# Kernel tuning notes

Measured on AMD Instinct MI355X. Metric: run time of the kernel, lower is better.

## Reference

```python
import jax, jax.numpy as jnp
import numpy as np

B, T, E = 4, 2048, 1024
H, D = 16, 64

def setup_inputs() -> dict:
    key = jax.random.key(0)
    k0, k1, k2, k3 = jax.random.split(key, 4)
    x = jax.random.normal(k0, (B, T, E), dtype=jnp.float32)
    Wq = jax.random.normal(k1, (H, E, D), dtype=jnp.float32) * (E ** -0.5)
    Wk = jax.random.normal(k2, (H, E, D), dtype=jnp.float32) * (E ** -0.5)
    Wv = jax.random.normal(k3, (H, E, D), dtype=jnp.float32) * (E ** -0.5)
    return {"x": x, "Wq": Wq, "Wk": Wk, "Wv": Wv}

def reference(x, Wq, Wk, Wv):
    # per-head projections: [B,T,E] x [H,E,D] -> [B,H,T,D]
    q = jnp.einsum('bte,hed->bhtd', x, Wq)
    k = jnp.einsum('bte,hed->bhtd', x, Wk)
    v = jnp.einsum('bte,hed->bhtd', x, Wv)
    d = q.shape[-1]
    scores = jnp.einsum('bhtd,bhsd->bhts', q, k) / jnp.sqrt(jnp.asarray(d, q.dtype))
    Tlen = x.shape[1]
    causal = jnp.tril(jnp.ones((Tlen, Tlen), dtype=bool))
    scores = jnp.where(causal, scores, -jnp.inf)
    weights = jax.nn.softmax(scores, axis=-1)
    out = jnp.einsum('bhts,bhsd->bhtd', weights, v)  # [B,H,T,D]
    # concat heads along last dim (head order preserved like torch.cat)
    Bb, Hh, Tt, Dd = out.shape
    return out.transpose(0, 2, 1, 3).reshape(Bb, Tt, Hh * Dd)
```

## Files before the change

kernel.cpp:

```cpp
#include <hip/hip_runtime.h>
#include <hip/hip_bf16.h>

#define BATCH 4
#define SEQ   2048
#define EMB   1024
#define NH    16
#define HD    64

#define Q_OFF  ((size_t)0)
#define K_OFF  ((size_t)8388608)
#define V_OFF  ((size_t)16777216)
#define WT_OFF ((size_t)25165824)

typedef __attribute__((ext_vector_type(8))) short short8;
typedef __attribute__((ext_vector_type(4))) short short4v;
typedef __attribute__((ext_vector_type(4))) float f32x4;

__device__ __forceinline__ short8 pack8s(float4 a, float4 b, float s) {
    alignas(16) __hip_bfloat16 t[8] = {
        __float2bfloat16(a.x * s), __float2bfloat16(a.y * s),
        __float2bfloat16(a.z * s), __float2bfloat16(a.w * s),
        __float2bfloat16(b.x * s), __float2bfloat16(b.y * s),
        __float2bfloat16(b.z * s), __float2bfloat16(b.w * s)};
    return *reinterpret_cast<const short8*>(t);
}

__device__ __forceinline__ void async16(void* lds, const void* g) {
    __builtin_amdgcn_global_load_lds(
        (const __attribute__((address_space(1))) unsigned int*)g,
        (__attribute__((address_space(3))) unsigned int*)lds, 16, 0, 0);
}

__global__ __launch_bounds__(256)
void xcast_kernel(const float* __restrict__ x, __hip_bfloat16* __restrict__ xb)
{
    const size_t i = ((size_t)blockIdx.x * 256 + threadIdx.x) * 8;
    float4 f0 = ((const float4*)(x + i))[0];
    float4 f1 = ((const float4*)(x + i))[1];
    *(short8*)(xb + i) = pack8s(f0, f1, 1.0f);
}

__global__ __launch_bounds__(256)
void wt_kernel(const float* __restrict__ Wq, const float* __restrict__ Wk,
               const float* __restrict__ Wv, __hip_bfloat16* __restrict__ Wt)
{
    const int et = blockIdx.x;
    const int mh = blockIdx.y;
    const int m = mh >> 4, h = mh & 15;
    const float* W = ((m == 0) ? Wq : (m == 1) ? Wk : Wv) + (size_t)h * (EMB * HD);
    const float scale = (m == 0) ? 0.18033688011112042f : 1.0f;

    __shared__ __hip_bfloat16 T[64][72];
    const int tid = threadIdx.x;
    const int r   = tid >> 2;
    const int seg = (tid & 3) * 16;

    {
        const float* src = W + (size_t)(et * 64 + r) * HD + seg;
        float4 f0 = ((const float4*)src)[0];
        float4 f1 = ((const float4*)src)[1];
        float4 f2 = ((const float4*)src)[2];
        float4 f3 = ((const float4*)src)[3];
        const float v[16] = {f0.x,f0.y,f0.z,f0.w, f1.x,f1.y,f1.z,f1.w,
                             f2.x,f2.y,f2.z,f2.w, f3.x,f3.y,f3.z,f3.w};
        #pragma unroll
        for (int j = 0; j < 16; ++j) T[seg + j][r] = __float2bfloat16(v[j] * scale);
    }
    __syncthreads();
    __hip_bfloat16* dst = Wt + ((size_t)mh * HD + r) * EMB + et * 64 + seg;
    *(short8*)dst       = *(const short8*)&T[r][seg];
    *(short8*)(dst + 8) = *(const short8*)&T[r][seg + 8];
}

__global__ __launch_bounds__(256)
void qkv_proj_kernel(const __hip_bfloat16* __restrict__ xb,
                     const __hip_bfloat16* __restrict__ Wt,
                     __hip_bfloat16* __restrict__ qkv)
{
    const int nt = blockIdx.x;
    const int rt = blockIdx.y;
    const int row0 = rt * 128;
    const int n0   = nt * 128;

    __shared__ __hip_bfloat16 lds[17408];
    __hip_bfloat16* As = lds;
    __hip_bfloat16* Bs = lds + 8192;

    const int tid  = threadIdx.x;
    const int wave = tid >> 6;
    const int lane = tid & 63;
    const int lr   = lane & 15;
    const int lg   = lane >> 4;

    const int srow  = lane >> 3;
    const int sslot = (lane & 7) ^ srow;
    const char* aSrc = (const char*)xb + (size_t)(row0 + wave * 32 + srow) * 2048 + sslot * 16;
    const char* bSrc = (const char*)Wt + (size_t)(n0   + wave * 32 + srow) * 2048 + sslot * 16;
    char* aDst = (char*)As + (size_t)(wave * 32) * 128;
    char* bDst = (char*)Bs + (size_t)(wave * 32) * 128;

    f32x4 acc[2][8] = {};

    for (int k0 = 0; k0 < EMB; k0 += 64) {
        __syncthreads();
        #pragma unroll
        for (int i = 0; i < 4; ++i) {
            async16(aDst + i * 1024, aSrc + (size_t)i * 16384 + k0 * 2);
            async16(bDst + i * 1024, bSrc + (size_t)i * 16384 + k0 * 2);
        }
        __syncthreads();

        #pragma unroll
        for (int half = 0; half < 2; ++half) {
            const int cg = half * 4 + lg;
            const int r0a = wave * 32 + lr;
            const int r1a = wave * 32 + 16 + lr;
            short8 a0 = *(const short8*)((char*)As + r0a * 128 + ((cg ^ (r0a & 7)) * 16));
            short8 a1 = *(const short8*)((char*)As + r1a * 128 + ((cg ^ (r1a & 7)) * 16));
            #pragma unroll
            for (int ct = 0; ct < 8; ++ct) {
                const int rb = ct * 16 + lr;
                short8 bf = *(const short8*)((char*)Bs + rb * 128 + ((cg ^ (rb & 7)) * 16));
                acc[0][ct] = __builtin_amdgcn_mfma_f32_16x16x32_bf16(a0, bf, acc[0][ct], 0, 0, 0);
                acc[1][ct] = __builtin_amdgcn_mfma_f32_16x16x32_bf16(a1, bf, acc[1][ct], 0, 0, 0);
            }
        }
    }

    const int m   = n0 >> 10;
    const int b   = row0 >> 11;
    const int tl0 = (row0 & (SEQ - 1)) + wave * 32;
    if (m < 2) {
        __hip_bfloat16* outp = qkv + ((m == 0) ? Q_OFF : K_OFF)
                             + (size_t)b * NH * SEQ * HD;
        #pragma unroll
        for (int rsub = 0; rsub < 2; ++rsub)
            #pragma unroll
            for (int ct = 0; ct < 8; ++ct) {
                const int h = (2 * nt + (ct >> 2)) & 15;
                const int d = (ct & 3) * 16 + lr;
                #pragma unroll
                for (int i = 0; i < 4; ++i) {
                    const int trow = tl0 + rsub * 16 + lg * 4 + i;
                    outp[((size_t)h * SEQ + trow) * HD + d] = __float2bfloat16(acc[rsub][ct][i]);
                }
            }
    } else {
        __hip_bfloat16 (*Ts)[136] = (__hip_bfloat16(*)[136])lds;
        __syncthreads();
        #pragma unroll
        for (int rsub = 0; rsub < 2; ++rsub)
            #pragma unroll
            for (int ct = 0; ct < 8; ++ct)
                #pragma unroll
                for (int i = 0; i < 4; ++i)
                    Ts[ct * 16 + lr][wave * 32 + rsub * 16 + lg * 4 + i] =
                        __float2bfloat16(acc[rsub][ct][i]);
        __syncthreads();
        const int c    = tid >> 1;
        const int tseg = (tid & 1) * 64;
        const int hv   = (2 * nt + (c >> 6)) & 15;
        const int dv   = c & 63;
        __hip_bfloat16* dst = qkv + V_OFF + ((size_t)b * NH + hv) * (HD * SEQ)
                            + (size_t)dv * SEQ + (row0 & (SEQ - 1)) + tseg;
        #pragma unroll
        for (int q = 0; q < 8; ++q)
            *(short8*)(dst + q * 8) = *(const short8*)&Ts[c][tseg + q * 8];
    }
}

__global__ __launch_bounds__(256)
void attn_kernel(const __hip_bfloat16* __restrict__ ws, float* __restrict__ out)
{
    const int bid     = blockIdx.x;
    const int logical = (bid & 7) * 64 + (bid >> 3);
    const int p  = logical & 7;
    const int h  = (logical >> 3) & 15;
    const int b  = logical >> 7;

    const __hip_bfloat16* qp = ws + Q_OFF + ((size_t)b * NH + h) * (SEQ * HD);
    const __hip_bfloat16* kp = ws + K_OFF + ((size_t)b * NH + h) * (SEQ * HD);
    const __hip_bfloat16* vt = ws + V_OFF + ((size_t)b * NH + h) * (HD * SEQ);

    __shared__ __align__(16) __hip_bfloat16 Ksb[2][4096];
    __shared__ __align__(16) __hip_bfloat16 Vsb[2][4096];
    __shared__ __align__(16) __hip_bfloat16 Psb[4][1024];

    const int tid  = threadIdx.x;
    const int wave = tid >> 6;
    const int lane = tid & 63;
    const int lr   = lane & 15;
    const int lg   = lane >> 4;
    const int l7   = lr & 7;

    const int srow8 = lane >> 3;
    const int sslot = (lane & 7) ^ srow8;

    float* op = out + (size_t)b * SEQ * (NH * HD) + (size_t)h * HD;

    for (int seg = 0; seg < 2; ++seg) {
        const int qt    = seg ? (15 - p) : p;
        const int qbase = qt * 128;
        const int ktmax = 2 * qt + 1;

        short8 qf[2][2];
        #pragma unroll
        for (int rsub = 0; rsub < 2; ++rsub) {
            const __hip_bfloat16* src =
                qp + (size_t)(qbase + wave * 32 + rsub * 16 + lr) * HD + lg * 8;
            qf[rsub][0] = *(const short8*)src;
            qf[rsub][1] = *(const short8*)(src + 32);
        }

        float m_run[2] = {-1e30f, -1e30f};
        float l_run[2] = {0.f, 0.f};
        f32x4 o_acc[2][4] = {};

        auto stage = [&](int buf, int kbase) {
            #pragma unroll
            for (int j = 0; j < 2; ++j) {
                const int r0 = wave * 16 + j * 8;
                async16((char*)Ksb[buf] + r0 * 128,
                        (const char*)(kp + (size_t)(kbase + r0 + srow8) * HD) + sslot * 16);
                async16((char*)Vsb[buf] + r0 * 128,
                        (const char*)(vt + (size_t)(r0 + srow8) * SEQ + kbase) + sslot * 16);
            }
        };

        stage(0, 0);
        __syncthreads();

        for (int kt = 0; kt <= ktmax; ++kt) {
            const int cur = kt & 1;
            if (kt < ktmax) stage(cur ^ 1, (kt + 1) * 64);

            f32x4 s[2][4];
            __builtin_amdgcn_s_setprio(1);
            #pragma unroll
            for (int ct = 0; ct < 4; ++ct) {
                const char* kb = (const char*)Ksb[cur] + (ct * 16 + lr) * 128;
                short8 kf0 = *(const short8*)(kb + ((lg      ^ l7) << 4));
                short8 kf1 = *(const short8*)(kb + (((lg + 4) ^ l7) << 4));
                #pragma unroll
                for (int rsub = 0; rsub < 2; ++rsub) {
                    f32x4 z = {};
                    z           = __builtin_amdgcn_mfma_f32_16x16x32_bf16(kf0, qf[rsub][0], z, 0, 0, 0);
                    s[rsub][ct] = __builtin_amdgcn_mfma_f32_16x16x32_bf16(kf1, qf[rsub][1], z, 0, 0, 0);
                }
            }
            __builtin_amdgcn_s_setprio(0);

            const int kbase = kt * 64;
            if (kt >= 2 * qt) {
                #pragma unroll
                for (int rsub = 0; rsub < 2; ++rsub) {
                    const int qrow = qbase + wave * 32 + rsub * 16 + lr;
                    #pragma unroll
                    for (int ct = 0; ct < 4; ++ct)
                        #pragma unroll
                        for (int i = 0; i < 4; ++i) {
                            const int key = kbase + ct * 16 + lg * 4 + i;
                            s[rsub][ct][i] = (key > qrow) ? -1e30f : s[rsub][ct][i];
                        }
                }
            }

            #pragma unroll
            for (int rsub = 0; rsub < 2; ++rsub) {
                float pmax = fmaxf(
                    fmaxf(fmaxf(fmaxf(s[rsub][0][0], s[rsub][0][1]), fmaxf(s[rsub][0][2], s[rsub][0][3])),
                          fmaxf(fmaxf(s[rsub][1][0], s[rsub][1][1]), fmaxf(s[rsub][1][2], s[rsub][1][3]))),
                    fmaxf(fmaxf(fmaxf(s[rsub][2][0], s[rsub][2][1]), fmaxf(s[rsub][2][2], s[rsub][2][3])),
                          fmaxf(fmaxf(s[rsub][3][0], s[rsub][3][1]), fmaxf(s[rsub][3][2], s[rsub][3][3]))));
                pmax = fmaxf(pmax, __shfl_xor(pmax, 16, 64));
                pmax = fmaxf(pmax, __shfl_xor(pmax, 32, 64));

                if (__any(pmax > m_run[rsub] + 8.0f)) {
                    const float mnew = fmaxf(m_run[rsub], pmax);
                    const float corr = __builtin_amdgcn_exp2f(m_run[rsub] - mnew);
                    l_run[rsub] *= corr;
                    #pragma unroll
                    for (int ct = 0; ct < 4; ++ct)
                        #pragma unroll
                        for (int i = 0; i < 4; ++i)
                            o_acc[rsub][ct][i] *= corr;
                    m_run[rsub] = mnew;
                }

                const float mcur = m_run[rsub];
                float rs0 = 0.f, rs1 = 0.f;
                #pragma unroll
                for (int ct = 0; ct < 4; ++ct) {
                    const float p0 = __builtin_amdgcn_exp2f(s[rsub][ct][0] - mcur);
                    const float p1 = __builtin_amdgcn_exp2f(s[rsub][ct][1] - mcur);
                    const float p2 = __builtin_amdgcn_exp2f(s[rsub][ct][2] - mcur);
                    const float p3 = __builtin_amdgcn_exp2f(s[rsub][ct][3] - mcur);
                    rs0 += p0 + p1;
                    rs1 += p2 + p3;
                    alignas(8) __hip_bfloat16 t[4] = {
                        __float2bfloat16(p0), __float2bfloat16(p1),
                        __float2bfloat16(p2), __float2bfloat16(p3)};
                    *(short4v*)((char*)Psb[wave] + lr * 128
                        + (((2 * ct + (lg >> 1)) ^ l7) << 4) + 8 * (lg & 1)) = *(const short4v*)t;
                }
                float rs = rs0 + rs1;
                rs += __shfl_xor(rs, 16, 64);
                rs += __shfl_xor(rs, 32, 64);
                l_run[rsub] += rs;

                const char* pb = (const char*)Psb[wave] + lr * 128;
                short8 pf0 = *(const short8*)(pb + ((lg      ^ l7) << 4));
                short8 pf1 = *(const short8*)(pb + (((lg + 4) ^ l7) << 4));
                __builtin_amdgcn_s_setprio(1);
                #pragma unroll
                for (int ct = 0; ct < 4; ++ct) {
                    const char* vb = (const char*)Vsb[cur] + (ct * 16 + lr) * 128;
                    short8 vf0 = *(const short8*)(vb + ((lg      ^ l7) << 4));
                    short8 vf1 = *(const short8*)(vb + (((lg + 4) ^ l7) << 4));
                    o_acc[rsub][ct] = __builtin_amdgcn_mfma_f32_16x16x32_bf16(vf0, pf0, o_acc[rsub][ct], 0, 0, 0);
                    o_acc[rsub][ct] = __builtin_amdgcn_mfma_f32_16x16x32_bf16(vf1, pf1, o_acc[rsub][ct], 0, 0, 0);
                }
                __builtin_amdgcn_s_setprio(0);
            }

            __syncthreads();
        }

        #pragma unroll
        for (int rsub = 0; rsub < 2; ++rsub) {
            const float inv  = 1.0f / l_run[rsub];
            const int   trow = qbase + wave * 32 + rsub * 16 + lr;
            #pragma unroll
            for (int ct = 0; ct < 4; ++ct) {
                float4 o;
                o.x = o_acc[rsub][ct][0] * inv;
                o.y = o_acc[rsub][ct][1] * inv;
                o.z = o_acc[rsub][ct][2] * inv;
                o.w = o_acc[rsub][ct][3] * inv;
                *(float4*)&op[(size_t)trow * (NH * HD) + ct * 16 + lg * 4] = o;
            }
        }
    }
}

extern "C" void kernel_launch(void* const* d_in, const int* in_sizes, int n_in,
                              void* d_out, int out_size, void* d_ws, size_t ws_size,
                              hipStream_t stream) {
    const float* x  = (const float*)d_in[0];
    const float* Wq = (const float*)d_in[1];
    const float* Wk = (const float*)d_in[2];
    const float* Wv = (const float*)d_in[3];
    float* out = (float*)d_out;
    __hip_bfloat16* ws = (__hip_bfloat16*)d_ws;

    __hip_bfloat16* xb = (__hip_bfloat16*)d_out;

    hipLaunchKernelGGL(xcast_kernel, dim3((BATCH * SEQ * EMB) / (256 * 8)), dim3(256),
                       0, stream, x, xb);
    hipLaunchKernelGGL(wt_kernel, dim3(16, 48), dim3(256), 0, stream,
                       Wq, Wk, Wv, ws + WT_OFF);
    hipLaunchKernelGGL(qkv_proj_kernel, dim3(24, 64), dim3(256), 0, stream,
                       xb, ws + WT_OFF, ws);
    hipLaunchKernelGGL(attn_kernel, dim3(512), dim3(256), 0, stream, ws, out);
}
```

Baseline: 157.3 us.

## Load K/V fragments directly from global memory and give each block one query tile

The attention kernel drops the double-buffered LDS staging of K and V tiles and the per-tile __syncthreads. Each wave now loads its MFMA fragments straight from global memory into registers. The grid doubles to 1024 blocks, each handling a single 128-row query tile with the longest tiles scheduled first, replacing the paired short/long segment scheme. This removes block-wide barriers and LDS traffic, but each wave now issues redundant global/L2 loads of the same K/V data, latency is no longer hidden by async prefetch, and register pressure rises.

Measured after the change: 261.6 us. 1.66x slower.

```diff
diff --git a/kernel.cpp b/kernel.cpp
--- a/kernel.cpp
+++ b/kernel.cpp
@@ -173,18 +173,19 @@
 void attn_kernel(const __hip_bfloat16* __restrict__ ws, float* __restrict__ out)
 {
     const int bid     = blockIdx.x;
-    const int logical = (bid & 7) * 64 + (bid >> 3);
-    const int p  = logical & 7;
-    const int h  = (logical >> 3) & 15;
-    const int b  = logical >> 7;
-
-    const __hip_bfloat16* qp = ws + Q_OFF + ((size_t)b * NH + h) * (SEQ * HD);
-    const __hip_bfloat16* kp = ws + K_OFF + ((size_t)b * NH + h) * (SEQ * HD);
-    const __hip_bfloat16* vt = ws + V_OFF + ((size_t)b * NH + h) * (HD * SEQ);
-
-    __shared__ __align__(16) __hip_bfloat16 Ksb[2][4096];
-    __shared__ __align__(16) __hip_bfloat16 Vsb[2][4096];
-    __shared__ __align__(16) __hip_bfloat16 Psb[4][1024];
+    const int logical = (bid & 7) * 128 + (bid >> 3);
+    const int qt = 15 - (logical & 15);
+    const int bh = logical >> 4;
+    const int h  = bh & 15;
+    const int b  = bh >> 4;
+    const int qbase = qt * 128;
+    const int ktmax = 2 * qt + 1;
+
+    const __hip_bfloat16* qp = ws + Q_OFF + (size_t)bh * (SEQ * HD);
+    const __hip_bfloat16* kp = ws + K_OFF + (size_t)bh * (SEQ * HD);
+    const __hip_bfloat16* vt = ws + V_OFF + (size_t)bh * (HD * SEQ);
+
+    __shared__ __align__(16) __hip_bfloat16 Psb[4][2][1024];
 
     const int tid  = threadIdx.x;
     const int wave = tid >> 6;
@@ -193,152 +194,142 @@
     const int lg   = lane >> 4;
     const int l7   = lr & 7;
 
-    const int srow8 = lane >> 3;
-    const int sslot = (lane & 7) ^ srow8;
+    short8 qf[2][2];
+    #pragma unroll
+    for (int rsub = 0; rsub < 2; ++rsub) {
+        const __hip_bfloat16* src =
+            qp + (size_t)(qbase + wave * 32 + rsub * 16 + lr) * HD + lg * 8;
+        qf[rsub][0] = *(const short8*)src;
+        qf[rsub][1] = *(const short8*)(src + 32);
+    }
+
+    float m_run[2] = {-1e30f, -1e30f};
+    float l_run[2] = {0.f, 0.f};
+    f32x4 o_acc[2][4] = {};
+
+    const __hip_bfloat16* kfp = kp + (size_t)(lr) * HD + lg * 8;
+    const __hip_bfloat16* vfp = vt + (size_t)(lr) * SEQ + lg * 8;
+
+    for (int kt = 0; kt <= ktmax; ++kt) {
+        const int kbase = kt * 64;
+
+        short8 kf[4][2];
+        #pragma unroll
+        for (int ct = 0; ct < 4; ++ct) {
+            const __hip_bfloat16* kb = kfp + (size_t)(kbase + ct * 16) * HD;
+            kf[ct][0] = *(const short8*)kb;
+            kf[ct][1] = *(const short8*)(kb + 32);
+        }
+
+        f32x4 s[2][4];
+        __builtin_amdgcn_s_setprio(1);
+        #pragma unroll
+        for (int ct = 0; ct < 4; ++ct)
+            #pragma unroll
+            for (int rsub = 0; rsub < 2; ++rsub) {
+                f32x4 z = {};
+                z           = __builtin_amdgcn_mfma_f32_16x16x32_bf16(kf[ct][0], qf[rsub][0], z, 0, 0, 0);
+                s[rsub][ct] = __builtin_amdgcn_mfma_f32_16x16x32_bf16(kf[ct][1], qf[rsub][1], z, 0, 0, 0);
+            }
+        __builtin_amdgcn_s_setprio(0);
+
+        short8 vf[4][2];
+        #pragma unroll
+        for (int ct = 0; ct < 4; ++ct) {
+            const __hip_bfloat16* vb = vfp + (size_t)(ct * 16) * SEQ + kbase;
+            vf[ct][0] = *(const short8*)vb;
+            vf[ct][1] = *(const short8*)(vb + 32);
+        }
+
+        if (kt >= 2 * qt) {
+            #pragma unroll
+            for (int rsub = 0; rsub < 2; ++rsub) {
+                const int qrow = qbase + wave * 32 + rsub * 16 + lr;
+                #pragma unroll
+                for (int ct = 0; ct < 4; ++ct)
+                    #pragma unroll
+                    for (int i = 0; i < 4; ++i) {
+                        const int key = kbase + ct * 16 + lg * 4 + i;
+                        s[rsub][ct][i] = (key > qrow) ? -1e30f : s[rsub][ct][i];
+                    }
+            }
+        }
+
+        #pragma unroll
+        for (int rsub = 0; rsub < 2; ++rsub) {
+            float pmax = fmaxf(
+                fmaxf(fmaxf(fmaxf(s[rsub][0][0], s[rsub][0][1]), fmaxf(s[rsub][0][2], s[rsub][0][3])),
+                      fmaxf(fmaxf(s[rsub][1][0], s[rsub][1][1]), fmaxf(s[rsub][1][2], s[rsub][1][3]))),
+                fmaxf(fmaxf(fmaxf(s[rsub][2][0], s[rsub][2][1]), fmaxf(s[rsub][2][2], s[rsub][2][3])),
+                      fmaxf(fmaxf(s[rsub][3][0], s[rsub][3][1]), fmaxf(s[rsub][3][2], s[rsub][3][3]))));
+            pmax = fmaxf(pmax, __shfl_xor(pmax, 16, 64));
+            pmax = fmaxf(pmax, __shfl_xor(pmax, 32, 64));
+
+            if (__any(pmax > m_run[rsub] + 8.0f)) {
+                const float mnew = fmaxf(m_run[rsub], pmax);
+                const float corr = __builtin_amdgcn_exp2f(m_run[rsub] - mnew);
+                l_run[rsub] *= corr;
+                #pragma unroll
+                for (int ct = 0; ct < 4; ++ct)
+                    #pragma unroll
+                    for (int i = 0; i < 4; ++i)
+                        o_acc[rsub][ct][i] *= corr;
+                m_run[rsub] = mnew;
+            }
+
+            const float mcur = m_run[rsub];
+            float rs0 = 0.f, rs1 = 0.f;
+            #pragma unroll
+            for (int ct = 0; ct < 4; ++ct) {
+                const float p0 = __builtin_amdgcn_exp2f(s[rsub][ct][0] - mcur);
+                const float p1 = __builtin_amdgcn_exp2f(s[rsub][ct][1] - mcur);
+                const float p2 = __builtin_amdgcn_exp2f(s[rsub][ct][2] - mcur);
+                const float p3 = __builtin_amdgcn_exp2f(s[rsub][ct][3] - mcur);
+                rs0 += p0 + p1;
+                rs1 += p2 + p3;
+                alignas(8) __hip_bfloat16 t[4] = {
+                    __float2bfloat16(p0), __float2bfloat16(p1),
+                    __float2bfloat16(p2), __float2bfloat16(p3)};
+                *(short4v*)((char*)Psb[wave][rsub] + lr * 128
+                    + (((2 * ct + (lg >> 1)) ^ l7) << 4) + 8 * (lg & 1)) = *(const short4v*)t;
+            }
+            float rs = rs0 + rs1;
+            rs += __shfl_xor(rs, 16, 64);
+            rs += __shfl_xor(rs, 32, 64);
+            l_run[rsub] += rs;
+        }
+
+        short8 pf[2][2];
+        #pragma unroll
+        for (int rsub = 0; rsub < 2; ++rsub) {
+            const char* pb = (const char*)Psb[wave][rsub] + lr * 128;
+            pf[rsub][0] = *(const short8*)(pb + ((lg      ^ l7) << 4));
+            pf[rsub][1] = *(const short8*)(pb + (((lg + 4) ^ l7) << 4));
+        }
+        __builtin_amdgcn_s_setprio(1);
+        #pragma unroll
+        for (int ct = 0; ct < 4; ++ct)
+            #pragma unroll
+            for (int rsub = 0; rsub < 2; ++rsub) {
+                o_acc[rsub][ct] = __builtin_amdgcn_mfma_f32_16x16x32_bf16(vf[ct][0], pf[rsub][0], o_acc[rsub][ct], 0, 0, 0);
+                o_acc[rsub][ct] = __builtin_amdgcn_mfma_f32_16x16x32_bf16(vf[ct][1], pf[rsub][1], o_acc[rsub][ct], 0, 0, 0);
+            }
+        __builtin_amdgcn_s_setprio(0);
+    }
 
     float* op = out + (size_t)b * SEQ * (NH * HD) + (size_t)h * HD;
-
-    for (int seg = 0; seg < 2; ++seg) {
-        const int qt    = seg ? (15 - p) : p;
-        const int qbase = qt * 128;
-        const int ktmax = 2 * qt + 1;
-
-        short8 qf[2][2];
-        #pragma unroll
-        for (int rsub = 0; rsub < 2; ++rsub) {
-            const __hip_bfloat16* src =
-                qp + (size_t)(qbase + wave * 32 + rsub * 16 + lr) * HD + lg * 8;
-            qf[rsub][0] = *(const short8*)src;
-            qf[rsub][1] = *(const short8*)(src + 32);
-        }
-
-        float m_run[2] = {-1e30f, -1e30f};
-        float l_run[2] = {0.f, 0.f};
-        f32x4 o_acc[2][4] = {};
-
-        auto stage = [&](int buf, int kbase) {
-            #pragma unroll
-            for (int j = 0; j < 2; ++j) {
-                const int r0 = wave * 16 + j * 8;
-                async16((char*)Ksb[buf] + r0 * 128,
-                        (const char*)(kp + (size_t)(kbase + r0 + srow8) * HD) + sslot * 16);
-                async16((char*)Vsb[buf] + r0 * 128,
-                        (const char*)(vt + (size_t)(r0 + srow8) * SEQ + kbase) + sslot * 16);
-            }
-        };
-
-        stage(0, 0);
-        __syncthreads();
-
-        for (int kt = 0; kt <= ktmax; ++kt) {
-            const int cur = kt & 1;
-            if (kt < ktmax) stage(cur ^ 1, (kt + 1) * 64);
-
-            f32x4 s[2][4];
-            __builtin_amdgcn_s_setprio(1);
-            #pragma unroll
-            for (int ct = 0; ct < 4; ++ct) {
-                const char* kb = (const char*)Ksb[cur] + (ct * 16 + lr) * 128;
-                short8 kf0 = *(const short8*)(kb + ((lg      ^ l7) << 4));
-                short8 kf1 = *(const short8*)(kb + (((lg + 4) ^ l7) << 4));
-                #pragma unroll
-                for (int rsub = 0; rsub < 2; ++rsub) {
-                    f32x4 z = {};
-                    z           = __builtin_amdgcn_mfma_f32_16x16x32_bf16(kf0, qf[rsub][0], z, 0, 0, 0);
-                    s[rsub][ct] = __builtin_amdgcn_mfma_f32_16x16x32_bf16(kf1, qf[rsub][1], z, 0, 0, 0);
-                }
-            }
-            __builtin_amdgcn_s_setprio(0);
-
-            const int kbase = kt * 64;
-            if (kt >= 2 * qt) {
-                #pragma unroll
-                for (int rsub = 0; rsub < 2; ++rsub) {
-                    const int qrow = qbase + wave * 32 + rsub * 16 + lr;
-                    #pragma unroll
-                    for (int ct = 0; ct < 4; ++ct)
-                        #pragma unroll
-                        for (int i = 0; i < 4; ++i) {
-                            const int key = kbase + ct * 16 + lg * 4 + i;
-                            s[rsub][ct][i] = (key > qrow) ? -1e30f : s[rsub][ct][i];
-                        }
-                }
-            }
-
-            #pragma unroll
-            for (int rsub = 0; rsub < 2; ++rsub) {
-                float pmax = fmaxf(
-                    fmaxf(fmaxf(fmaxf(s[rsub][0][0], s[rsub][0][1]), fmaxf(s[rsub][0][2], s[rsub][0][3])),
-                          fmaxf(fmaxf(s[rsub][1][0], s[rsub][1][1]), fmaxf(s[rsub][1][2], s[rsub][1][3]))),
-                    fmaxf(fmaxf(fmaxf(s[rsub][2][0], s[rsub][2][1]), fmaxf(s[rsub][2][2], s[rsub][2][3])),
-                          fmaxf(fmaxf(s[rsub][3][0], s[rsub][3][1]), fmaxf(s[rsub][3][2], s[rsub][3][3]))));
-                pmax = fmaxf(pmax, __shfl_xor(pmax, 16, 64));
-                pmax = fmaxf(pmax, __shfl_xor(pmax, 32, 64));
-
-                if (__any(pmax > m_run[rsub] + 8.0f)) {
-                    const float mnew = fmaxf(m_run[rsub], pmax);
-                    const float corr = __builtin_amdgcn_exp2f(m_run[rsub] - mnew);
-                    l_run[rsub] *= corr;
-                    #pragma unroll
-                    for (int ct = 0; ct < 4; ++ct)
-                        #pragma unroll
-                        for (int i = 0; i < 4; ++i)
-                            o_acc[rsub][ct][i] *= corr;
-                    m_run[rsub] = mnew;
-                }
-
-                const float mcur = m_run[rsub];
-                float rs0 = 0.f, rs1 = 0.f;
-                #pragma unroll
-                for (int ct = 0; ct < 4; ++ct) {
-                    const float p0 = __builtin_amdgcn_exp2f(s[rsub][ct][0] - mcur);
-                    const float p1 = __builtin_amdgcn_exp2f(s[rsub][ct][1] - mcur);
-                    const float p2 = __builtin_amdgcn_exp2f(s[rsub][ct][2] - mcur);
-                    const float p3 = __builtin_amdgcn_exp2f(s[rsub][ct][3] - mcur);
-                    rs0 += p0 + p1;
-                    rs1 += p2 + p3;
-                    alignas(8) __hip_bfloat16 t[4] = {
-                        __float2bfloat16(p0), __float2bfloat16(p1),
-                        __float2bfloat16(p2), __float2bfloat16(p3)};
-                    *(short4v*)((char*)Psb[wave] + lr * 128
-                        + (((2 * ct + (lg >> 1)) ^ l7) << 4) + 8 * (lg & 1)) = *(const short4v*)t;
-                }
-                float rs = rs0 + rs1;
-                rs += __shfl_xor(rs, 16, 64);
-                rs += __shfl_xor(rs, 32, 64);
-                l_run[rsub] += rs;
-
-                const char* pb = (const char*)Psb[wave] + lr * 128;
-                short8 pf0 = *(const short8*)(pb + ((lg      ^ l7) << 4));
-                short8 pf1 = *(const short8*)(pb + (((lg + 4) ^ l7) << 4));
-                __builtin_amdgcn_s_setprio(1);
-                #pragma unroll
-                for (int ct = 0; ct < 4; ++ct) {
-                    const char* vb = (const char*)Vsb[cur] + (ct * 16 + lr) * 128;
-                    short8 vf0 = *(const short8*)(vb + ((lg      ^ l7) << 4));
-                    short8 vf1 = *(const short8*)(vb + (((lg + 4) ^ l7) << 4));
-                    o_acc[rsub][ct] = __builtin_amdgcn_mfma_f32_16x16x32_bf16(vf0, pf0, o_acc[rsub][ct], 0, 0, 0);
-                    o_acc[rsub][ct] = __builtin_amdgcn_mfma_f32_16x16x32_bf16(vf1, pf1, o_acc[rsub][ct], 0, 0, 0);
-                }
-                __builtin_amdgcn_s_setprio(0);
-            }
-
-            __syncthreads();
-        }
-
-        #pragma unroll
-        for (int rsub = 0; rsub < 2; ++rsub) {
-            const float inv  = 1.0f / l_run[rsub];
-            const int   trow = qbase + wave * 32 + rsub * 16 + lr;
-            #pragma unroll
-            for (int ct = 0; ct < 4; ++ct) {
-                float4 o;
-                o.x = o_acc[rsub][ct][0] * inv;
-                o.y = o_acc[rsub][ct][1] * inv;
-                o.z = o_acc[rsub][ct][2] * inv;
-                o.w = o_acc[rsub][ct][3] * inv;
-                *(float4*)&op[(size_t)trow * (NH * HD) + ct * 16 + lg * 4] = o;
-            }
+    #pragma unroll
+    for (int rsub = 0; rsub < 2; ++rsub) {
+        const float inv  = 1.0f / l_run[rsub];
+        const int   trow = qbase + wave * 32 + rsub * 16 + lr;
+        #pragma unroll
+        for (int ct = 0; ct < 4; ++ct) {
+            float4 o;
+            o.x = o_acc[rsub][ct][0] * inv;
+            o.y = o_acc[rsub][ct][1] * inv;
+            o.z = o_acc[rsub][ct][2] * inv;
+            o.w = o_acc[rsub][ct][3] * inv;
+            *(float4*)&op[(size_t)trow * (NH * HD) + ct * 16 + lg * 4] = o;
         }
     }
 }
@@ -361,5 +352,5 @@
                        Wq, Wk, Wv, ws + WT_OFF);
     hipLaunchKernelGGL(qkv_proj_kernel, dim3(24, 64), dim3(256), 0, stream,
                        xb, ws + WT_OFF, ws);
-    hipLaunchKernelGGL(attn_kernel, dim3(512), dim3(256), 0, stream, ws, out);
-}
+    hipLaunchKernelGGL(attn_kernel, dim3(1024), dim3(256), 0, stream, ws, out);
+}
```

## Launch one attention block per query tile, heaviest first, and batch PV MFMAs

Applied to the files above, without the earlier changes.

Replaces the paired-segment scheme (each of 512 blocks processing two complementary query tiles) with 1024 blocks, each handling one 128-row query tile. Tiles are ordered longest-first so the hardware scheduler can balance the causal workload dynamically. The P tile is now staged per rsub, so both rows' PV MFMAs run together and each V fragment loaded from LDS is reused twice. This adds more block launches and doubles the per-wave P buffer in LDS, which may reduce occupancy.

After: 182.8 us. 16.2% more time.

```diff
diff --git a/kernel.cpp b/kernel.cpp
--- a/kernel.cpp
+++ b/kernel.cpp
@@ -173,18 +173,21 @@
 void attn_kernel(const __hip_bfloat16* __restrict__ ws, float* __restrict__ out)
 {
     const int bid     = blockIdx.x;
-    const int logical = (bid & 7) * 64 + (bid >> 3);
-    const int p  = logical & 7;
-    const int h  = (logical >> 3) & 15;
-    const int b  = logical >> 7;
-
-    const __hip_bfloat16* qp = ws + Q_OFF + ((size_t)b * NH + h) * (SEQ * HD);
-    const __hip_bfloat16* kp = ws + K_OFF + ((size_t)b * NH + h) * (SEQ * HD);
-    const __hip_bfloat16* vt = ws + V_OFF + ((size_t)b * NH + h) * (HD * SEQ);
+    const int logical = (bid & 7) * 128 + (bid >> 3);
+    const int qt = 15 - (logical & 15);
+    const int bh = logical >> 4;
+    const int h  = bh & 15;
+    const int b  = bh >> 4;
+    const int qbase = qt * 128;
+    const int ktmax = 2 * qt + 1;
+
+    const __hip_bfloat16* qp = ws + Q_OFF + (size_t)bh * (SEQ * HD);
+    const __hip_bfloat16* kp = ws + K_OFF + (size_t)bh * (SEQ * HD);
+    const __hip_bfloat16* vt = ws + V_OFF + (size_t)bh * (HD * SEQ);
 
     __shared__ __align__(16) __hip_bfloat16 Ksb[2][4096];
     __shared__ __align__(16) __hip_bfloat16 Vsb[2][4096];
-    __shared__ __align__(16) __hip_bfloat16 Psb[4][1024];
+    __shared__ __align__(16) __hip_bfloat16 Psb[4][2][1024];
 
     const int tid  = threadIdx.x;
     const int wave = tid >> 6;
@@ -196,149 +199,149 @@
     const int srow8 = lane >> 3;
     const int sslot = (lane & 7) ^ srow8;
 
+    short8 qf[2][2];
+    #pragma unroll
+    for (int rsub = 0; rsub < 2; ++rsub) {
+        const __hip_bfloat16* src =
+            qp + (size_t)(qbase + wave * 32 + rsub * 16 + lr) * HD + lg * 8;
+        qf[rsub][0] = *(const short8*)src;
+        qf[rsub][1] = *(const short8*)(src + 32);
+    }
+
+    float m_run[2] = {-1e30f, -1e30f};
+    float l_run[2] = {0.f, 0.f};
+    f32x4 o_acc[2][4] = {};
+
+    auto stage = [&](int buf, int kbase) {
+        #pragma unroll
+        for (int j = 0; j < 2; ++j) {
+            const int r0 = wave * 16 + j * 8;
+            async16((char*)Ksb[buf] + r0 * 128,
+                    (const char*)(kp + (size_t)(kbase + r0 + srow8) * HD) + sslot * 16);
+            async16((char*)Vsb[buf] + r0 * 128,
+                    (const char*)(vt + (size_t)(r0 + srow8) * SEQ + kbase) + sslot * 16);
+        }
+    };
+
+    stage(0, 0);
+    __syncthreads();
+
+    for (int kt = 0; kt <= ktmax; ++kt) {
+        const int cur = kt & 1;
+        if (kt < ktmax) stage(cur ^ 1, (kt + 1) * 64);
+
+        f32x4 s[2][4];
+        __builtin_amdgcn_s_setprio(1);
+        #pragma unroll
+        for (int ct = 0; ct < 4; ++ct) {
+            const char* kb = (const char*)Ksb[cur] + (ct * 16 + lr) * 128;
+            short8 kf0 = *(const short8*)(kb + ((lg      ^ l7) << 4));
+            short8 kf1 = *(const short8*)(kb + (((lg + 4) ^ l7) << 4));
+            #pragma unroll
+            for (int rsub = 0; rsub < 2; ++rsub) {
+                f32x4 z = {};
+                z           = __builtin_amdgcn_mfma_f32_16x16x32_bf16(kf0, qf[rsub][0], z, 0, 0, 0);
+                s[rsub][ct] = __builtin_amdgcn_mfma_f32_16x16x32_bf16(kf1, qf[rsub][1], z, 0, 0, 0);
+            }
+        }
+        __builtin_amdgcn_s_setprio(0);
+
+        const int kbase = kt * 64;
+        if (kt >= 2 * qt) {
+            #pragma unroll
+            for (int rsub = 0; rsub < 2; ++rsub) {
+                const int qrow = qbase + wave * 32 + rsub * 16 + lr;
+                #pragma unroll
+                for (int ct = 0; ct < 4; ++ct)
+                    #pragma unroll
+                    for (int i = 0; i < 4; ++i) {
+                        const int key = kbase + ct * 16 + lg * 4 + i;
+                        s[rsub][ct][i] = (key > qrow) ? -1e30f : s[rsub][ct][i];
+                    }
+            }
+        }
+
+        #pragma unroll
+        for (int rsub = 0; rsub < 2; ++rsub) {
+            float pmax = fmaxf(
+                fmaxf(fmaxf(fmaxf(s[rsub][0][0], s[rsub][0][1]), fmaxf(s[rsub][0][2], s[rsub][0][3])),
+                      fmaxf(fmaxf(s[rsub][1][0], s[rsub][1][1]), fmaxf(s[rsub][1][2], s[rsub][1][3]))),
+                fmaxf(fmaxf(fmaxf(s[rsub][2][0], s[rsub][2][1]), fmaxf(s[rsub][2][2], s[rsub][2][3])),
+                      fmaxf(fmaxf(s[rsub][3][0], s[rsub][3][1]), fmaxf(s[rsub][3][2], s[rsub][3][3]))));
+            pmax = fmaxf(pmax, __shfl_xor(pmax, 16, 64));
+            pmax = fmaxf(pmax, __shfl_xor(pmax, 32, 64));
+
+            if (__any(pmax > m_run[rsub] + 8.0f)) {
+                const float mnew = fmaxf(m_run[rsub], pmax);
+                const float corr = __builtin_amdgcn_exp2f(m_run[rsub] - mnew);
+                l_run[rsub] *= corr;
+                #pragma unroll
+                for (int ct = 0; ct < 4; ++ct)
+                    #pragma unroll
+                    for (int i = 0; i < 4; ++i)
+                        o_acc[rsub][ct][i] *= corr;
+                m_run[rsub] = mnew;
+            }
+
+            const float mcur = m_run[rsub];
+            float rs0 = 0.f, rs1 = 0.f;
+            #pragma unroll
+            for (int ct = 0; ct < 4; ++ct) {
+                const float p0 = __builtin_amdgcn_exp2f(s[rsub][ct][0] - mcur);
+                const float p1 = __builtin_amdgcn_exp2f(s[rsub][ct][1] - mcur);
+                const float p2 = __builtin_amdgcn_exp2f(s[rsub][ct][2] - mcur);
+                const float p3 = __builtin_amdgcn_exp2f(s[rsub][ct][3] - mcur);
+                rs0 += p0 + p1;
+                rs1 += p2 + p3;
+                alignas(8) __hip_bfloat16 t[4] = {
+                    __float2bfloat16(p0), __float2bfloat16(p1),
+                    __float2bfloat16(p2), __float2bfloat16(p3)};
+                *(short4v*)((char*)Psb[wave][rsub] + lr * 128
+                    + (((2 * ct + (lg >> 1)) ^ l7) << 4) + 8 * (lg & 1)) = *(const short4v*)t;
+            }
+            float rs = rs0 + rs1;
+            rs += __shfl_xor(rs, 16, 64);
+            rs += __shfl_xor(rs, 32, 64);
+            l_run[rsub] += rs;
+        }
+
+        short8 pf[2][2];
+        #pragma unroll
+        for (int rsub = 0; rsub < 2; ++rsub) {
+            const char* pb = (const char*)Psb[wave][rsub] + lr * 128;
+            pf[rsub][0] = *(const short8*)(pb + ((lg      ^ l7) << 4));
+            pf[rsub][1] = *(const short8*)(pb + (((lg + 4) ^ l7) << 4));
+        }
+        __builtin_amdgcn_s_setprio(1);
+        #pragma unroll
+        for (int ct = 0; ct < 4; ++ct) {
+            const char* vb = (const char*)Vsb[cur] + (ct * 16 + lr) * 128;
+            short8 vf0 = *(const short8*)(vb + ((lg      ^ l7) << 4));
+            short8 vf1 = *(const short8*)(vb + (((lg + 4) ^ l7) << 4));
+            #pragma unroll
+            for (int rsub = 0; rsub < 2; ++rsub) {
+                o_acc[rsub][ct] = __builtin_amdgcn_mfma_f32_16x16x32_bf16(vf0, pf[rsub][0], o_acc[rsub][ct], 0, 0, 0);
+                o_acc[rsub][ct] = __builtin_amdgcn_mfma_f32_16x16x32_bf16(vf1, pf[rsub][1], o_acc[rsub][ct], 0, 0, 0);
+            }
+        }
+        __builtin_amdgcn_s_setprio(0);
+
+        __syncthreads();
+    }
+
     float* op = out + (size_t)b * SEQ * (NH * HD) + (size_t)h * HD;
-
-    for (int seg = 0; seg < 2; ++seg) {
-        const int qt    = seg ? (15 - p) : p;
-        const int qbase = qt * 128;
-        const int ktmax = 2 * qt + 1;
-
-        short8 qf[2][2];
-        #pragma unroll
-        for (int rsub = 0; rsub < 2; ++rsub) {
-            const __hip_bfloat16* src =
-                qp + (size_t)(qbase + wave * 32 + rsub * 16 + lr) * HD + lg * 8;
-            qf[rsub][0] = *(const short8*)src;
-            qf[rsub][1] = *(const short8*)(src + 32);
-        }
-
-        float m_run[2] = {-1e30f, -1e30f};
-        float l_run[2] = {0.f, 0.f};
-        f32x4 o_acc[2][4] = {};
-
-        auto stage = [&](int buf, int kbase) {
-            #pragma unroll
-            for (int j = 0; j < 2; ++j) {
-                const int r0 = wave * 16 + j * 8;
-                async16((char*)Ksb[buf] + r0 * 128,
-                        (const char*)(kp + (size_t)(kbase + r0 + srow8) * HD) + sslot * 16);
-                async16((char*)Vsb[buf] + r0 * 128,
-                        (const char*)(vt + (size_t)(r0 + srow8) * SEQ + kbase) + sslot * 16);
-            }
-        };
-
-        stage(0, 0);
-        __syncthreads();
-
-        for (int kt = 0; kt <= ktmax; ++kt) {
-            const int cur = kt & 1;
-            if (kt < ktmax) stage(cur ^ 1, (kt + 1) * 64);
-
-            f32x4 s[2][4];
-            __builtin_amdgcn_s_setprio(1);
-            #pragma unroll
-            for (int ct = 0; ct < 4; ++ct) {
-                const char* kb = (const char*)Ksb[cur] + (ct * 16 + lr) * 128;
-                short8 kf0 = *(const short8*)(kb + ((lg      ^ l7) << 4));
-                short8 kf1 = *(const short8*)(kb + (((lg + 4) ^ l7) << 4));
-                #pragma unroll
-                for (int rsub = 0; rsub < 2; ++rsub) {
-                    f32x4 z = {};
-                    z           = __builtin_amdgcn_mfma_f32_16x16x32_bf16(kf0, qf[rsub][0], z, 0, 0, 0);
-                    s[rsub][ct] = __builtin_amdgcn_mfma_f32_16x16x32_bf16(kf1, qf[rsub][1], z, 0, 0, 0);
-                }
-            }
-            __builtin_amdgcn_s_setprio(0);
-
-            const int kbase = kt * 64;
-            if (kt >= 2 * qt) {
-                #pragma unroll
-                for (int rsub = 0; rsub < 2; ++rsub) {
-                    const int qrow = qbase + wave * 32 + rsub * 16 + lr;
-                    #pragma unroll
-                    for (int ct = 0; ct < 4; ++ct)
-                        #pragma unroll
-                        for (int i = 0; i < 4; ++i) {
-                            const int key = kbase + ct * 16 + lg * 4 + i;
-                            s[rsub][ct][i] = (key > qrow) ? -1e30f : s[rsub][ct][i];
-                        }
-                }
-            }
-
-            #pragma unroll
-            for (int rsub = 0; rsub < 2; ++rsub) {
-                float pmax = fmaxf(
-                    fmaxf(fmaxf(fmaxf(s[rsub][0][0], s[rsub][0][1]), fmaxf(s[rsub][0][2], s[rsub][0][3])),
-                          fmaxf(fmaxf(s[rsub][1][0], s[rsub][1][1]), fmaxf(s[rsub][1][2], s[rsub][1][3]))),
-                    fmaxf(fmaxf(fmaxf(s[rsub][2][0], s[rsub][2][1]), fmaxf(s[rsub][2][2], s[rsub][2][3])),
-                          fmaxf(fmaxf(s[rsub][3][0], s[rsub][3][1]), fmaxf(s[rsub][3][2], s[rsub][3][3]))));
-                pmax = fmaxf(pmax, __shfl_xor(pmax, 16, 64));
-                pmax = fmaxf(pmax, __shfl_xor(pmax, 32, 64));
-
-                if (__any(pmax > m_run[rsub] + 8.0f)) {
-                    const float mnew = fmaxf(m_run[rsub], pmax);
-                    const float corr = __builtin_amdgcn_exp2f(m_run[rsub] - mnew);
-                    l_run[rsub] *= corr;
-                    #pragma unroll
-                    for (int ct = 0; ct < 4; ++ct)
-                        #pragma unroll
-                        for (int i = 0; i < 4; ++i)
-                            o_acc[rsub][ct][i] *= corr;
-                    m_run[rsub] = mnew;
-                }
-
-                const float mcur = m_run[rsub];
-                float rs0 = 0.f, rs1 = 0.f;
-                #pragma unroll
-                for (int ct = 0; ct < 4; ++ct) {
-                    const float p0 = __builtin_amdgcn_exp2f(s[rsub][ct][0] - mcur);
-                    const float p1 = __builtin_amdgcn_exp2f(s[rsub][ct][1] - mcur);
-                    const float p2 = __builtin_amdgcn_exp2f(s[rsub][ct][2] - mcur);
-                    const float p3 = __builtin_amdgcn_exp2f(s[rsub][ct][3] - mcur);
-                    rs0 += p0 + p1;
-                    rs1 += p2 + p3;
-                    alignas(8) __hip_bfloat16 t[4] = {
-                        __float2bfloat16(p0), __float2bfloat16(p1),
-                        __float2bfloat16(p2), __float2bfloat16(p3)};
-                    *(short4v*)((char*)Psb[wave] + lr * 128
-                        + (((2 * ct + (lg >> 1)) ^ l7) << 4) + 8 * (lg & 1)) = *(const short4v*)t;
-                }
-                float rs = rs0 + rs1;
-                rs += __shfl_xor(rs, 16, 64);
-                rs += __shfl_xor(rs, 32, 64);
-                l_run[rsub] += rs;
-
-                const char* pb = (const char*)Psb[wave] + lr * 128;
-                short8 pf0 = *(const short8*)(pb + ((lg      ^ l7) << 4));
-                short8 pf1 = *(const short8*)(pb + (((lg + 4) ^ l7) << 4));
-                __builtin_amdgcn_s_setprio(1);
-                #pragma unroll
-                for (int ct = 0; ct < 4; ++ct) {
-                    const char* vb = (const char*)Vsb[cur] + (ct * 16 + lr) * 128;
-                    short8 vf0 = *(const short8*)(vb + ((lg      ^ l7) << 4));
-                    short8 vf1 = *(const short8*)(vb + (((lg + 4) ^ l7) << 4));
-                    o_acc[rsub][ct] = __builtin_amdgcn_mfma_f32_16x16x32_bf16(vf0, pf0, o_acc[rsub][ct], 0, 0, 0);
-                    o_acc[rsub][ct] = __builtin_amdgcn_mfma_f32_16x16x32_bf16(vf1, pf1, o_acc[rsub][ct], 0, 0, 0);
-                }
-                __builtin_amdgcn_s_setprio(0);
-            }
-
-            __syncthreads();
-        }
-
-        #pragma unroll
-        for (int rsub = 0; rsub < 2; ++rsub) {
-            const float inv  = 1.0f / l_run[rsub];
-            const int   trow = qbase + wave * 32 + rsub * 16 + lr;
-            #pragma unroll
-            for (int ct = 0; ct < 4; ++ct) {
-                float4 o;
-                o.x = o_acc[rsub][ct][0] * inv;
-                o.y = o_acc[rsub][ct][1] * inv;
-                o.z = o_acc[rsub][ct][2] * inv;
-                o.w = o_acc[rsub][ct][3] * inv;
-                *(float4*)&op[(size_t)trow * (NH * HD) + ct * 16 + lg * 4] = o;
-            }
+    #pragma unroll
+    for (int rsub = 0; rsub < 2; ++rsub) {
+        const float inv  = 1.0f / l_run[rsub];
+        const int   trow = qbase + wave * 32 + rsub * 16 + lr;
+        #pragma unroll
+        for (int ct = 0; ct < 4; ++ct) {
+            float4 o;
+            o.x = o_acc[rsub][ct][0] * inv;
+            o.y = o_acc[rsub][ct][1] * inv;
+            o.z = o_acc[rsub][ct][2] * inv;
+            o.w = o_acc[rsub][ct][3] * inv;
+            *(float4*)&op[(size_t)trow * (NH * HD) + ct * 16 + lg * 4] = o;
         }
     }
 }
@@ -361,5 +364,5 @@
                        Wq, Wk, Wv, ws + WT_OFF);
     hipLaunchKernelGGL(qkv_proj_kernel, dim3(24, 64), dim3(256), 0, stream,
                        xb, ws + WT_OFF, ws);
-    hipLaunchKernelGGL(attn_kernel, dim3(512), dim3(256), 0, stream, ws, out);
-}
+    hipLaunchKernelGGL(attn_kernel, dim3(1024), dim3(256), 0, stream, ws, out);
+}
```
